# Kernel optimization log

Hardware: AMD Instinct MI355X
Metric: run time of the kernel (lower is better)

The kernel has to match this reference:

```python
import jax, jax.numpy as jnp
import numpy as np

T = 4096; D = 768; V = 32000; L = 4; EPS = 1e-5


def _ln(x, g, b):
    m = jnp.mean(x, axis=-1, keepdims=True)
    v = jnp.mean((x - m) ** 2, axis=-1, keepdims=True)
    return (x - m) * jax.lax.rsqrt(v + EPS) * g + b


def _qgelu(x):
    return x * jax.nn.sigmoid(1.702 * x)


def setup_inputs() -> dict:
    key = jax.random.key(0)
    ks = jax.random.split(key, 10)
    s = 0.02
    return {
        "idx": jax.random.randint(ks[0], (T,), 0, V),
        "wte": jax.random.normal(ks[1], (V, D)) * s,
        "rb_ln_g": jnp.ones((D,)), "rb_ln_b": jnp.zeros((D,)),
        "rb_fc_w": jax.random.normal(ks[2], (D, 4 * D)) * s,
        "rb_fc_b": jnp.zeros((4 * D,)),
        "rb_proj_w": jax.random.normal(ks[3], (4 * D, D)) * s,
        "rb_proj_b": jnp.zeros((D,)),
        "lnf_g": jnp.ones((D,)), "lnf_b": jnp.zeros((D,)),
        "lm_head_w": jax.random.normal(ks[4], (D, V)) * s,
        "mb_ln_g": jnp.ones((L, 2 * D)), "mb_ln_b": jnp.zeros((L, 2 * D)),
        "mb_fc_w": jax.random.normal(ks[5], (L, 2 * D, 4 * D)) * s,
        "mb_fc_b": jnp.zeros((L, 4 * D)),
        "mb_proj_w": jax.random.normal(ks[6], (L, 4 * D, D)) * s,
        "mb_proj_b": jnp.zeros((L, D)),
        "op_w": jax.random.normal(ks[7], (L, D, D)) * s,
        "op_b": jnp.zeros((L, D)),
        "lns_g": jnp.ones((L, D)), "lns_b": jnp.zeros((L, D)),
        "heads_w": jax.random.normal(ks[8], (L, D, V)) * s,
    }


def reference(idx, wte, rb_ln_g, rb_ln_b, rb_fc_w, rb_fc_b, rb_proj_w, rb_proj_b,
              lnf_g, lnf_b, lm_head_w, mb_ln_g, mb_ln_b, mb_fc_w, mb_fc_b,
              mb_proj_w, mb_proj_b, op_w, op_b, lns_g, lns_b, heads_w):
    # token embedding (dropout is identity in eval) + initial residual block
    x = wte[idx]  # [T, D]
    h = _ln(x, rb_ln_g, rb_ln_b)
    x = x + _qgelu(h @ rb_fc_w + rb_fc_b) @ rb_proj_w + rb_proj_b
    x = _ln(x, lnf_g, lnf_b)
    logits = x @ lm_head_w  # [T, V]

    # targets=None path: pred_targets = cat(idx[1:], [-1])
    pred_targets = jnp.concatenate([idx[1:], jnp.full((1,), -1, idx.dtype)])
    pos = jnp.arange(T)
    skey = jax.random.key(42)

    for i in range(L):  # static small loop over layers
        j = i + 1
        # multinomial(softmax(logits), 1) == categorical(logits)
        idx_next = jax.random.categorical(jax.random.fold_in(skey, i), logits)
        # positions p where the sample matched the next-token target and p < T - j
        mask = (idx_next == pred_targets) & (pos < T - j)  # [T] bool
        # x2[p] = x[p + j] (padded); compute merge densely, select with mask
        x2 = jnp.concatenate([x[j:], jnp.zeros((j, D), x.dtype)], axis=0)
        h = _ln(jnp.concatenate([x, x2], axis=-1), mb_ln_g[i], mb_ln_b[i])
        merged = x2 + _qgelu(h @ mb_fc_w[i] + mb_fc_b[i]) @ mb_proj_w[i] + mb_proj_b[i]
        # scatter merged[p] into x at position p + j where mask[p]
        merged_s = jnp.concatenate([jnp.zeros((j, D), x.dtype), merged[:-j]], axis=0)
        mask_s = jnp.concatenate([jnp.zeros((j,), bool), mask[:-j]], axis=0)
        x = jnp.where(mask_s[:, None], merged_s, x)
        x = x @ op_w[i] + op_b[i]
        x = _ln(x, lns_g[i], lns_b[i])
        logits = x @ heads_w[i]
    return logits
```

## Files before the change

### kernel.cpp

```cpp
#include <hip/hip_runtime.h>
#include <cstdint>
#include <cstddef>

#define T_TOK 4096
#define DIM   768
#define VOCAB 32000
#define NLAYER 4
#define HALF_TV 65536000u

typedef short bf16x8 __attribute__((ext_vector_type(8)));
typedef float f32x4  __attribute__((ext_vector_type(4)));
typedef float f32x4v __attribute__((ext_vector_type(4)));

__host__ __device__ inline void tf2x32(uint32_t k0, uint32_t k1, uint32_t& v0, uint32_t& v1){
  uint32_t ks2 = k0 ^ k1 ^ 0x1BD11BDAu;
  uint32_t x0 = v0 + k0, x1 = v1 + k1;
#define TFR(R) { x0 += x1; x1 = (x1<<R)|(x1>>(32-R)); x1 ^= x0; }
  TFR(13) TFR(15) TFR(26) TFR(6)
  x0 += k1;  x1 += ks2 + 1u;
  TFR(17) TFR(29) TFR(16) TFR(24)
  x0 += ks2; x1 += k0 + 2u;
  TFR(13) TFR(15) TFR(26) TFR(6)
  x0 += k0;  x1 += k1 + 3u;
  TFR(17) TFR(29) TFR(16) TFR(24)
  x0 += k1;  x1 += ks2 + 4u;
  TFR(13) TFR(15) TFR(26) TFR(6)
  x0 += ks2; x1 += k0 + 5u;
#undef TFR
  v0 = x0; v1 = x1;
}

__device__ inline float neglog_u(uint32_t k){
  float L;
  if (k >= 0x780000u){
    float x = (float)(0x800000u - k) * 1.1920928955078125e-7f;
    L = x * fmaf(x, fmaf(x, fmaf(x, 0.25f, 0.3333333333333f), 0.5f), 1.0f);
  } else {
    float l2k = __builtin_amdgcn_logf((float)k);
    L = 0.69314718055994531f * (23.0f - l2k);
    if (k == 0u) L = 87.33654475055310898f;
  }
  return L;
}

__device__ inline void gumbel_pair(uint32_t kf0, uint32_t kf1, uint32_t t_up, uint32_t v,
                                   float& gu, float& gd){
  uint32_t m = t_up * (uint32_t)VOCAB + v;
  uint32_t x0 = m, x1 = m + HALF_TV;
  tf2x32(kf0, kf1, x0, x1);
  float Lu = neglog_u(x0 >> 9);
  float Ld = neglog_u(x1 >> 9);
  gu = -0.69314718055994531f * __builtin_amdgcn_logf(Lu);
  gd = -0.69314718055994531f * __builtin_amdgcn_logf(Ld);
}

__device__ inline unsigned short f2bf(float f){
  uint32_t u = __float_as_uint(f);
  return (unsigned short)((u + 0x7FFFu + ((u >> 16) & 1u)) >> 16);
}
__device__ inline float bf2f(unsigned short h){
  return __uint_as_float(((uint32_t)h) << 16);
}
__device__ inline void cvt8(const float* f, bool lo, unsigned short* out){
  #pragma unroll
  for (int e=0;e<8;e++){
    float x = f[e];
    unsigned short h = f2bf(x);
    if (lo) h = f2bf(x - bf2f(h));
    out[e] = h;
  }
}
__device__ inline float blockReduceSum(float v){
  __shared__ float red[4];
  #pragma unroll
  for (int off=32; off>0; off>>=1) v += __shfl_down(v, off);
  int w = threadIdx.x >> 6;
  __syncthreads();
  if ((threadIdx.x & 63) == 0) red[w] = v;
  __syncthreads();
  return red[0] + red[1] + red[2] + red[3];
}

__device__ inline void gload16(const void* g, void* l){
  __builtin_amdgcn_global_load_lds(
      (const __attribute__((address_space(1))) unsigned int*)g,
      (__attribute__((address_space(3))) unsigned int*)l, 16, 0, 0);
}

enum { ST_F32 = 0, ST_HILO = 1, ST_SAMPLE = 2 };

template<int KSTEPS, int NSEG, int STORE, bool NTST, bool BIAS, bool QGELU>
__global__ __launch_bounds__(1024, 4) void k_hgemm256(
    const unsigned short* __restrict__ A0, const unsigned short* __restrict__ A1,
    const unsigned short* __restrict__ B0, const unsigned short* __restrict__ B2,
    float* __restrict__ C, unsigned short* __restrict__ Ch, unsigned short* __restrict__ Cl,
    const float* __restrict__ bias, uint32_t kf0, uint32_t kf1,
    unsigned long long* __restrict__ row_best, int N)
{
  constexpr int K  = KSTEPS * 64;
  constexpr int NT = NSEG * KSTEPS;
  __shared__ unsigned short sAll[65536];

  const int t = threadIdx.x;
  const int w = t >> 6, l = t & 63;
  const int wm = w >> 2, wn = w & 3;
  const int g = l >> 4, r = l & 15;

  int bid = blockIdx.x;
  int xcd = bid & 7, c = bid >> 3;
  int bm = xcd*2 + (c & 1);
  int bn = c >> 1;

  f32x4 acc[4][4] = {};

  size_t arow[2], brow[2];
  #pragma unroll
  for (int p=0;p<2;p++){
    int mr = p*128 + (t >> 3);
    int blk = mr >> 4;
    arow[p] = (size_t)(bm*128 + ((blk>>1)<<4) + (mr & 15) + ((blk & 1) ? 2048 : 0)) * K;
    int nr = p*128 + (t >> 3);
    brow[p] = (size_t)(bn*256 + nr) * K;
  }
  const int swz  = ((t & 7) ^ ((t >> 3) & 7)) << 3;
  const int ldst = t * 16;

  auto stage = [&](int vt){
    char* base = (char*)sAll + (vt & 1) * 65536;
    int seg = (NSEG == 1) ? 0 : (vt / KSTEPS);
    int k0  = ((NSEG == 1) ? vt : (vt % KSTEPS)) * 64;
    const unsigned short* Ap = (seg == 1) ? A1 : A0;
    const unsigned short* Bp = (seg == 2) ? B2 : B0;
    #pragma unroll
    for (int p=0;p<2;p++)
      gload16(Ap + arow[p] + k0 + swz, base + p*16384 + ldst);
    #pragma unroll
    for (int p=0;p<2;p++)
      gload16(Bp + brow[p] + k0 + swz, base + 32768 + p*16384 + ldst);
  };

  stage(0);
  __syncthreads();

  for (int vt = 0; vt < NT; ++vt){
    if (vt + 1 < NT) stage(vt + 1);
    const char* sA = (const char*)sAll + (vt & 1) * 65536;
    const char* sB = sA + 32768;
    #pragma unroll
    for (int kk=0;kk<2;kk++){
      bf16x8 bv[4], av[4];
      #pragma unroll
      for (int ni=0;ni<4;ni++){
        int tr = wn*64 + ni*16 + r;
        bv[ni] = *(const bf16x8*)(sB + tr*128 + (((kk*4+g) ^ (r&7))<<4));
      }
      #pragma unroll
      for (int q=0;q<4;q++){
        int tr = wm*64 + q*16 + r;
        av[q] = *(const bf16x8*)(sA + tr*128 + (((kk*4+g) ^ (r&7))<<4));
      }
      __builtin_amdgcn_s_setprio(1);
      #pragma unroll
      for (int q=0;q<4;q++)
        #pragma unroll
        for (int ni=0;ni<4;ni++)
          acc[q][ni] = __builtin_amdgcn_mfma_f32_16x16x32_bf16(av[q], bv[ni], acc[q][ni], 0, 0, 0);
      __builtin_amdgcn_s_setprio(0);
    }
    __syncthreads();
  }

  if constexpr (STORE == ST_SAMPLE){
    #pragma unroll
    for (int mi=0; mi<4; mi+=2){
      int row16 = (wm*2 + (mi>>1)) * 16;
      #pragma unroll
      for (int jj=0;jj<4;jj++){
        uint32_t t_up = bm*128 + row16 + g*4 + jj;
        unsigned long long bu = 0ull, bd = 0ull;
        #pragma unroll
        for (int ni=0;ni<4;ni++){
          uint32_t v = bn*256 + wn*64 + ni*16 + r;
          float gu, gd;
          gumbel_pair(kf0, kf1, t_up, v, gu, gd);
          float vu = acc[mi][ni][jj]   + gu;
          float vd = acc[mi+1][ni][jj] + gd;
          uint32_t fu = __float_as_uint(vu); fu = (fu & 0x80000000u) ? ~fu : (fu | 0x80000000u);
          uint32_t fd = __float_as_uint(vd); fd = (fd & 0x80000000u) ? ~fd : (fd | 0x80000000u);
          unsigned long long pu = ((unsigned long long)fu << 32) | (unsigned long long)(~v);
          unsigned long long pd = ((unsigned long long)fd << 32) | (unsigned long long)(~v);
          if (pu > bu) bu = pu;
          if (pd > bd) bd = pd;
        }
        #pragma unroll
        for (int off=1; off<16; off<<=1){
          unsigned int l0 = (unsigned int)bu, h0 = (unsigned int)(bu>>32);
          unsigned int l1 = __shfl_xor(l0, off), h1 = __shfl_xor(h0, off);
          unsigned long long o = ((unsigned long long)h1 << 32) | (unsigned long long)l1;
          if (o > bu) bu = o;
          l0 = (unsigned int)bd; h0 = (unsigned int)(bd>>32);
          l1 = __shfl_xor(l0, off); h1 = __shfl_xor(h0, off);
          o = ((unsigned long long)h1 << 32) | (unsigned long long)l1;
          if (o > bd) bd = o;
        }
        if (r == 0){
          atomicMax(&row_best[t_up], bu);
          atomicMax(&row_best[t_up + 2048], bd);
        }
      }
    }
  } else {
    #pragma unroll
    for (int mi=0;mi<4;mi++){
      int blk = wm*4 + mi;
      int mbase = bm*128 + ((blk>>1)<<4) + ((blk & 1) ? 2048 : 0);
      #pragma unroll
      for (int ni=0;ni<4;ni++){
        int n = bn*256 + wn*64 + ni*16 + r;
        float bv_ = BIAS ? bias[n] : 0.0f;
        #pragma unroll
        for (int jj=0;jj<4;jj++){
          int m = mbase + g*4 + jj;
          float v = acc[mi][ni][jj] + bv_;
          if constexpr (QGELU) v = v / (1.0f + expf(-1.702f * v));
          if constexpr (STORE == ST_F32){
            if constexpr (NTST) __builtin_nontemporal_store(v, &C[(size_t)m * N + n]);
            else                C[(size_t)m * N + n] = v;
          } else {
            unsigned short h = f2bf(v);
            Ch[(size_t)m * N + n] = h;
            Cl[(size_t)m * N + n] = f2bf(v - bf2f(h));
          }
        }
      }
    }
  }
}

template<int KSTEPS, int NSEG, bool BIAS, bool QGELU, bool RES, int STORE>
__global__ __launch_bounds__(256) void k_hgemm(
    const unsigned short* __restrict__ A0, const unsigned short* __restrict__ A1,
    const unsigned short* __restrict__ B0, const unsigned short* __restrict__ B2,
    float* __restrict__ C, unsigned short* __restrict__ Ch, unsigned short* __restrict__ Cl,
    const float* __restrict__ bias, const float* __restrict__ res,
    int N, uint32_t kf0, uint32_t kf1, unsigned long long* __restrict__ row_best)
{
  constexpr int K  = KSTEPS * 64;
  constexpr int NT = NSEG * KSTEPS;
  __shared__ unsigned short sAll[2 * 16 * 1024];

  const int t = threadIdx.x;
  const int wave = t >> 6, lane = t & 63;
  const int wm = wave >> 1, wn = wave & 1;
  const int g = lane >> 4, r = lane & 15;
  const int lr = lane >> 3, lc = lane & 7;

  int bid = blockIdx.x;
  int xcd = bid & 7, c = bid >> 3;
  int bm = xcd*4 + (c & 3);
  int bn = c >> 2;

  f32x4 acc[4][4] = {};

  size_t arow[4], brow[4];
  #pragma unroll
  for (int p=0;p<4;p++){
    int mr = p*32 + wave*8 + lr;
    int blk = mr >> 4;
    arow[p] = (size_t)(bm*64 + ((blk>>1)<<4) + (mr & 15) + ((blk & 1) ? 2048 : 0)) * K;
    brow[p] = (size_t)(bn*128 + mr) * K;
  }
  const int swz  = (lc ^ lr) << 3;
  const int ldst = (wave*8 + lr)*128 + lc*16;

  auto stage = [&](int vt){
    char* base = (char*)sAll + (vt & 1) * 32768;
    int seg = (NSEG == 1) ? 0 : (vt / KSTEPS);
    int k0  = ((NSEG == 1) ? vt : (vt % KSTEPS)) * 64;
    const unsigned short* Ap = (seg == 1) ? A1 : A0;
    const unsigned short* Bp = (seg == 2) ? B2 : B0;
    #pragma unroll
    for (int p=0;p<4;p++){
      gload16(Ap + arow[p] + k0 + swz, base + p*4096 + ldst);
      gload16(Bp + brow[p] + k0 + swz, base + 16384 + p*4096 + ldst);
    }
  };

  stage(0);
  __syncthreads();

  for (int vt = 0; vt < NT; ++vt){
    if (vt + 1 < NT) stage(vt + 1);
    const char* sA = (const char*)sAll + (vt & 1) * 32768;
    const char* sB = sA + 16384;
    #pragma unroll
    for (int kk=0;kk<2;kk++){
      bf16x8 av[4], bv[4];
      #pragma unroll
      for (int mi=0;mi<4;mi++){
        int tr = wm*64 + mi*16 + r;
        av[mi] = *(const bf16x8*)(sA + tr*128 + (((kk*4+g) ^ (r&7))<<4));
      }
      #pragma unroll
      for (int ni=0;ni<4;ni++){
        int tr = wn*64 + ni*16 + r;
        bv[ni] = *(const bf16x8*)(sB + tr*128 + (((kk*4+g) ^ (r&7))<<4));
      }
      #pragma unroll
      for (int mi=0;mi<4;mi++)
        #pragma unroll
        for (int ni=0;ni<4;ni++)
          acc[mi][ni] = __builtin_amdgcn_mfma_f32_16x16x32_bf16(av[mi], bv[ni], acc[mi][ni], 0, 0, 0);
    }
    __syncthreads();
  }

  #pragma unroll
  for (int mi=0;mi<4;mi++){
    int blk2 = wm*4 + mi;
    int mbase = bm*64 + ((blk2>>1)<<4) + ((blk2 & 1) ? 2048 : 0);
    #pragma unroll
    for (int ni=0;ni<4;ni++){
      int n = bn*128 + wn*64 + ni*16 + r;
      float bv_ = BIAS ? bias[n] : 0.0f;
      #pragma unroll
      for (int jj=0;jj<4;jj++){
        int m = mbase + g*4 + jj;
        float v = acc[mi][ni][jj] + bv_;
        if constexpr (QGELU) v = v / (1.0f + expf(-1.702f * v));
        if constexpr (RES)   v += res[(size_t)m * N + n];
        if constexpr (STORE == ST_F32){
          C[(size_t)m * N + n] = v;
        } else {
          unsigned short h = f2bf(v);
          Ch[(size_t)m * N + n] = h;
          Cl[(size_t)m * N + n] = f2bf(v - bf2f(h));
        }
      }
    }
  }
}

template<bool SPLIT>
__global__ __launch_bounds__(256) void k_wt_t(const float* __restrict__ W,
    unsigned short* __restrict__ Bh, unsigned short* __restrict__ Bl, int K, int N)
{
  __shared__ unsigned short sH[64][72];
  __shared__ unsigned short sL[64][72];
  int kt = blockIdx.x, nt = blockIdx.y;
  int t = threadIdx.x;
  int kr = t >> 4, nc4 = (t & 15) * 4;
  #pragma unroll
  for (int p=0;p<4;p++){
    int k = p*16 + kr;
    f32x4v w = __builtin_nontemporal_load((const f32x4v*)&W[(size_t)(kt*64 + k) * N + nt*64 + nc4]);
    #pragma unroll
    for (int e=0;e<4;e++){
      unsigned short h = f2bf(w[e]);
      sH[nc4+e][k] = h;
      if (SPLIT) sL[nc4+e][k] = f2bf(w[e] - bf2f(h));
    }
  }
  __syncthreads();
  #pragma unroll
  for (int q=0;q<2;q++){
    int cid = t + q*256;
    int n = cid >> 3, ch = cid & 7;
    *(bf16x8*)&Bh[(size_t)(nt*64+n)*K + kt*64 + ch*8] = *(const bf16x8*)&sH[n][ch*8];
    if (SPLIT)
      *(bf16x8*)&Bl[(size_t)(nt*64+n)*K + kt*64 + ch*8] = *(const bf16x8*)&sL[n][ch*8];
  }
}

__global__ __launch_bounds__(256) void k_embed_ln(const int* __restrict__ idx,
    const float* __restrict__ wte, const float* __restrict__ g, const float* __restrict__ b,
    float* __restrict__ Xraw, unsigned short* __restrict__ Hh, unsigned short* __restrict__ Hl)
{
  int row = blockIdx.x;
  const float* src = wte + (size_t)idx[row] * DIM;
  float v[3];
  #pragma unroll
  for (int jj=0;jj<3;jj++) v[jj] = src[threadIdx.x + jj*256];
  float s = blockReduceSum(v[0]+v[1]+v[2]);
  float mean = s * (1.0f/DIM);
  float s2 = 0;
  #pragma unroll
  for (int jj=0;jj<3;jj++){ float d = v[jj]-mean; s2 += d*d; }
  s2 = blockReduceSum(s2);
  float rs = rsqrtf(s2 * (1.0f/DIM) + 1e-5f);
  #pragma unroll
  for (int jj=0;jj<3;jj++){
    int d = threadIdx.x + jj*256;
    Xraw[(size_t)row*DIM + d] = v[jj];
    float o = (v[jj]-mean)*rs*g[d] + b[d];
    unsigned short h = f2bf(o);
    Hh[(size_t)row*DIM + d] = h;
    Hl[(size_t)row*DIM + d] = f2bf(o - bf2f(h));
  }
}

__global__ __launch_bounds__(256) void k_ln(const float* __restrict__ in, float* __restrict__ out,
    const float* __restrict__ g, const float* __restrict__ b,
    unsigned short* __restrict__ obf, unsigned short* __restrict__ olo)
{
  int row = blockIdx.x;
  const float* src = in + (size_t)row * DIM;
  float v[3];
  #pragma unroll
  for (int jj=0;jj<3;jj++) v[jj] = src[threadIdx.x + jj*256];
  float s = blockReduceSum(v[0]+v[1]+v[2]);
  float mean = s * (1.0f/DIM);
  float s2 = 0;
  #pragma unroll
  for (int jj=0;jj<3;jj++){ float d = v[jj]-mean; s2 += d*d; }
  s2 = blockReduceSum(s2);
  float rs = rsqrtf(s2 * (1.0f/DIM) + 1e-5f);
  #pragma unroll
  for (int jj=0;jj<3;jj++){
    int d = threadIdx.x + jj*256;
    float o = (v[jj]-mean)*rs*g[d] + b[d];
    out[(size_t)row*DIM + d] = o;
    unsigned short h = f2bf(o);
    obf[(size_t)row*DIM + d] = h;
    olo[(size_t)row*DIM + d] = f2bf(o - bf2f(h));
  }
}

__global__ void k_mask(const unsigned long long* __restrict__ row_best,
    const int* __restrict__ idx, int j, int* __restrict__ count, int* __restrict__ plist)
{
  int t = blockIdx.x * blockDim.x + threadIdx.x;
  if (t >= T_TOK) return;
  int v = (int)(~(uint32_t)(row_best[t] & 0xFFFFFFFFull));
  int tgt = (t < T_TOK-1) ? idx[t+1] : -1;
  if (v == tgt && t < T_TOK - j){
    int pos = atomicAdd(count, 1);
    plist[pos] = t;
  }
}

__global__ __launch_bounds__(256) void k_merge(const float* __restrict__ X,
    const int* __restrict__ plist, const int* __restrict__ count,
    const float* __restrict__ lng, const float* __restrict__ lnb,
    const float* __restrict__ fcw, const float* __restrict__ fcb,
    const float* __restrict__ pjw, const float* __restrict__ pjb,
    float* __restrict__ mergebuf, int j)
{
  __shared__ float sh[1536 + 3072];
  int nb = *count;
  for (int bIdx = blockIdx.x; bIdx < nb; bIdx += gridDim.x){
    int p = plist[bIdx];
    const float* xp = X + (size_t)p * DIM;
    const float* x2 = X + (size_t)(p + j) * DIM;
    for (int d = threadIdx.x; d < 1536; d += 256)
      sh[d] = (d < DIM) ? xp[d] : x2[d - DIM];
    __syncthreads();
    float s = 0;
    for (int d = threadIdx.x; d < 1536; d += 256) s += sh[d];
    s = blockReduceSum(s);
    float mean = s * (1.0f/1536.0f);
    float s2 = 0;
    for (int d = threadIdx.x; d < 1536; d += 256){ float df = sh[d]-mean; s2 += df*df; }
    s2 = blockReduceSum(s2);
    float rs = rsqrtf(s2 * (1.0f/1536.0f) + 1e-5f);
    __syncthreads();
    for (int d = threadIdx.x; d < 1536; d += 256)
      sh[d] = (sh[d]-mean)*rs*lng[d] + lnb[d];
    __syncthreads();
    float* act = sh + 1536;
    #pragma unroll
    for (int jj=0;jj<12;jj++){
      int n = threadIdx.x + jj*256;
      float a = fcb[n];
      for (int k=0;k<1536;k++) a += sh[k]*fcw[(size_t)k*3072 + n];
      act[n] = a / (1.0f + expf(-1.702f*a));
    }
    __syncthreads();
    #pragma unroll
    for (int jj=0;jj<3;jj++){
      int d = threadIdx.x + jj*256;
      float a = pjb[d];
      for (int k=0;k<3072;k++) a += act[k]*pjw[(size_t)k*DIM + d];
      mergebuf[(size_t)bIdx*DIM + d] = x2[d] + a;
    }
    __syncthreads();
  }
}

__global__ void k_scatter(float* __restrict__ X, unsigned short* __restrict__ Xbf,
    unsigned short* __restrict__ Xlo, const float* __restrict__ mergebuf,
    const int* __restrict__ plist, const int* __restrict__ count, int j)
{
  int nb = *count;
  for (int bIdx = blockIdx.x; bIdx < nb; bIdx += gridDim.x){
    int p = plist[bIdx];
    for (int d = threadIdx.x; d < DIM; d += 256){
      float v = mergebuf[(size_t)bIdx*DIM + d];
      size_t o = (size_t)(p + j)*DIM + d;
      X[o] = v;
      unsigned short h = f2bf(v);
      Xbf[o] = h;
      Xlo[o] = f2bf(v - bf2f(h));
    }
  }
}

__global__ __launch_bounds__(256) void k_gemm_old(
    const float* __restrict__ A, const float* __restrict__ B, float* __restrict__ C,
    int M, int N, int K)
{
  __shared__ unsigned short sA[128*64];
  __shared__ unsigned short sB[128*64];
  const int t = threadIdx.x;
  const int bn = blockIdx.x, bm = blockIdx.y;
  const int wave = t >> 6, lane = t & 63;
  const int wm = wave >> 1, wn = wave & 1;
  const int g = lane >> 4, r = lane & 15;
  f32x4 acc[4][4] = {};
  const int nK = K >> 6;
  const int aC = t & 7,  aM0 = t >> 3;
  const int bN0 = t & 31, bC = t >> 5;
  const float* Abase = A + (size_t)(bm*128) * K;
  const float* Bbase = B + (size_t)(bn*128);
  for (int seg = 0; seg < 3; ++seg) {
    const bool aLO = (seg == 1), bLO = (seg == 2);
    for (int kb = 0; kb < nK; ++kb) {
      const int k0 = kb << 6;
      __syncthreads();
      #pragma unroll
      for (int p=0;p<4;p++){
        int m = p*32 + aM0;
        const float* src = Abase + (size_t)m * K + k0 + aC*8;
        float ff[8];
        *(float4*)(ff)   = *(const float4*)(src);
        *(float4*)(ff+4) = *(const float4*)(src+4);
        unsigned short hh[8];
        cvt8(ff, aLO, hh);
        *(bf16x8*)&sA[m*64 + ((aC ^ (m & 7)) * 8)] = *(bf16x8*)hh;
      }
      #pragma unroll
      for (int p=0;p<4;p++){
        int n = p*32 + bN0;
        float ff[8];
        const float* src = Bbase + (size_t)(k0 + bC*8) * N + n;
        #pragma unroll
        for (int e=0;e<8;e++) ff[e] = src[(size_t)e * N];
        unsigned short hh[8];
        cvt8(ff, bLO, hh);
        *(bf16x8*)&sB[n*64 + ((bC ^ (n & 7)) * 8)] = *(bf16x8*)hh;
      }
      __syncthreads();
      #pragma unroll
      for (int kk=0;kk<2;kk++){
        bf16x8 av[4], bv[4];
        #pragma unroll
        for (int mi=0;mi<4;mi++){
          int m = wm*64 + mi*16 + r;
          av[mi] = *(const bf16x8*)&sA[m*64 + (((kk*4 + g) ^ (m & 7)) * 8)];
        }
        #pragma unroll
        for (int ni=0;ni<4;ni++){
          int n = wn*64 + ni*16 + r;
          bv[ni] = *(const bf16x8*)&sB[n*64 + (((kk*4 + g) ^ (n & 7)) * 8)];
        }
        #pragma unroll
        for (int mi=0;mi<4;mi++)
          #pragma unroll
          for (int ni=0;ni<4;ni++)
            acc[mi][ni] = __builtin_amdgcn_mfma_f32_16x16x32_bf16(av[mi], bv[ni], acc[mi][ni], 0, 0, 0);
      }
    }
  }
  #pragma unroll
  for (int mi=0;mi<4;mi++)
    #pragma unroll
    for (int ni=0;ni<4;ni++)
      #pragma unroll
      for (int jj=0;jj<4;jj++){
        int m = bm*128 + wm*64 + mi*16 + g*4 + jj;
        int n = bn*128 + wn*64 + ni*16 + r;
        C[(size_t)m * N + n] = acc[mi][ni][jj];
      }
}

static void fold_key(uint32_t i, uint32_t& o0, uint32_t& o1){
  uint32_t x0 = 0, x1 = i;
  tf2x32(0u, 42u, x0, x1);
  o0 = x0; o1 = x1;
}

extern "C" void kernel_launch(void* const* d_in, const int* in_sizes, int n_in,
                              void* d_out, int out_size, void* d_ws, size_t ws_size,
                              hipStream_t stream)
{
  const int*   idx       = (const int*)  d_in[0];
  const float* wte       = (const float*)d_in[1];
  const float* rb_ln_g   = (const float*)d_in[2];
  const float* rb_ln_b   = (const float*)d_in[3];
  const float* rb_fc_w   = (const float*)d_in[4];
  const float* rb_fc_b   = (const float*)d_in[5];
  const float* rb_proj_w = (const float*)d_in[6];
  const float* rb_proj_b = (const float*)d_in[7];
  const float* lnf_g     = (const float*)d_in[8];
  const float* lnf_b     = (const float*)d_in[9];
  const float* lm_head_w = (const float*)d_in[10];
  const float* mb_ln_g   = (const float*)d_in[11];
  const float* mb_ln_b   = (const float*)d_in[12];
  const float* mb_fc_w   = (const float*)d_in[13];
  const float* mb_fc_b   = (const float*)d_in[14];
  const float* mb_proj_w = (const float*)d_in[15];
  const float* mb_proj_b = (const float*)d_in[16];
  const float* op_w      = (const float*)d_in[17];
  const float* op_b      = (const float*)d_in[18];
  const float* lns_g     = (const float*)d_in[19];
  const float* lns_b     = (const float*)d_in[20];
  const float* heads_w   = (const float*)d_in[21];

  const size_t TD = (size_t)T_TOK * DIM;
  const size_t DV = (size_t)DIM * VOCAB;

  float* X = (float*)d_ws;
  float* Y = X + TD;
  unsigned short* Xbf = (unsigned short*)(Y + TD);
  unsigned short* Xlo = Xbf + TD;
  unsigned short* BtFh = Xlo + TD;
  unsigned short* BtFl = BtFh + DV;
  size_t need_big = (size_t)((char*)(BtFl + DV) - (char*)d_ws);
  bool big = ws_size >= need_big;

  char* ob = (char*)d_out;
  float* OUT = (float*)d_out;
  unsigned short* Hh     = (unsigned short*)(ob);
  unsigned short* Hl     = Hh + TD;
  unsigned short* ACTh   = (unsigned short*)(ob + ((size_t)16<<20));
  unsigned short* ACTl   = ACTh + TD*4;
  unsigned short* Btfc_h = (unsigned short*)(ob + ((size_t)72<<20));
  unsigned short* Btfc_l = Btfc_h + (size_t)3072*DIM;
  unsigned short* Btpj_h = (unsigned short*)(ob + ((size_t)84<<20));
  unsigned short* Btpj_l = Btpj_h + (size_t)3072*DIM;
  unsigned short* BtS    = (unsigned short*)(ob + ((size_t)96<<20));
  unsigned short* Btop_h = (unsigned short*)(ob + ((size_t)152<<20));
  unsigned short* Btop_l = Btop_h + (size_t)DIM*DIM;
  float* MERGE = (float*)(ob + ((size_t)160<<20));
  unsigned long long* ROWBEST = (unsigned long long*)(ob + ((size_t)176<<20));
  int* COUNT = (int*)(ROWBEST + T_TOK);
  int* PLIST = COUNT + 1;

  dim3 blk(256);
  dim3 blk16(1024);

  k_embed_ln<<<T_TOK, blk, 0, stream>>>(idx, wte, rb_ln_g, rb_ln_b, X, Hh, Hl);
  k_wt_t<true><<<dim3(12,48), blk, 0, stream>>>(rb_fc_w,   Btfc_h, Btfc_l, DIM,  3072);
  k_wt_t<true><<<dim3(48,12), blk, 0, stream>>>(rb_proj_w, Btpj_h, Btpj_l, 3072, DIM);
  k_hgemm256<12,3,ST_HILO,false,true,true><<<16*12, blk16, 0, stream>>>(
      Hh, Hl, Btfc_h, Btfc_l, nullptr, ACTh, ACTl, rb_fc_b, 0u,0u, nullptr, 3072);
  k_hgemm<48,3,true,false,true,ST_F32><<<6*32, blk, 0, stream>>>(
      ACTh, ACTl, Btpj_h, Btpj_l, Y, nullptr, nullptr, rb_proj_b, X, DIM, 0u,0u, nullptr);
  k_ln<<<T_TOK, blk, 0, stream>>>(Y, X, lnf_g, lnf_b, Xbf, Xlo);

  for (int i = 0; i < NLAYER; ++i){
    int j = i + 1;
    uint32_t kf0, kf1; fold_key((uint32_t)i, kf0, kf1);

    hipMemsetAsync(ROWBEST, 0, (size_t)T_TOK*8 + 4, stream);

    const float* hw = (i == 0) ? lm_head_w : heads_w + (size_t)(i-1)*DV;
    k_wt_t<false><<<dim3(12,500), blk, 0, stream>>>(hw, BtS, nullptr, DIM, VOCAB);
    k_hgemm256<12,1,ST_SAMPLE,false,false,false><<<2000, blk16, 0, stream>>>(
        Xbf, Xbf, BtS, BtS, nullptr, nullptr, nullptr, nullptr, kf0, kf1, ROWBEST, VOCAB);

    k_mask<<<T_TOK/256, blk, 0, stream>>>(ROWBEST, idx, j, COUNT, PLIST);
    k_merge<<<64, blk, 0, stream>>>(X, PLIST, COUNT,
        mb_ln_g + (size_t)i*1536, mb_ln_b + (size_t)i*1536,
        mb_fc_w + (size_t)i*1536*3072, mb_fc_b + (size_t)i*3072,
        mb_proj_w + (size_t)i*3072*DIM, mb_proj_b + (size_t)i*DIM, MERGE, j);
    k_scatter<<<64, blk, 0, stream>>>(X, Xbf, Xlo, MERGE, PLIST, COUNT, j);

    k_wt_t<true><<<dim3(12,12), blk, 0, stream>>>(op_w + (size_t)i*DIM*DIM, Btop_h, Btop_l, DIM, DIM);
    k_hgemm<12,3,true,false,false,ST_F32><<<6*32, blk, 0, stream>>>(
        Xbf, Xlo, Btop_h, Btop_l, Y, nullptr, nullptr, op_b + (size_t)i*DIM, nullptr,
        DIM, 0u,0u, nullptr);
    k_ln<<<T_TOK, blk, 0, stream>>>(Y, X, lns_g + (size_t)i*DIM, lns_b + (size_t)i*DIM, Xbf, Xlo);
  }

  if (big){
    k_wt_t<true><<<dim3(12,500), blk, 0, stream>>>(heads_w + (size_t)3*DV, BtFh, BtFl, DIM, VOCAB);
    k_hgemm256<12,3,ST_F32,true,false,false><<<2000, blk16, 0, stream>>>(
        Xbf, Xlo, BtFh, BtFl, OUT, nullptr, nullptr, nullptr, 0u, 0u, nullptr, VOCAB);
  } else {
    k_gemm_old<<<dim3(VOCAB/128, T_TOK/128), blk, 0, stream>>>(
        X, heads_w + (size_t)3*DV, OUT, T_TOK, VOCAB, DIM);
  }
}
```

Before: 2.564 ms.

## Use 8-wave blocks with 128x64 warp tiles and barrier-interleaved MFMA phases

```diff
diff --git a/kernel.cpp b/kernel.cpp
--- a/kernel.cpp
+++ b/kernel.cpp
@@ -90,7 +90,7 @@
 enum { ST_F32 = 0, ST_HILO = 1, ST_SAMPLE = 2 };
 
 template<int KSTEPS, int NSEG, int STORE, bool NTST, bool BIAS, bool QGELU>
-__global__ __launch_bounds__(1024, 4) void k_hgemm256(
+__global__ __launch_bounds__(512, 2) void k_hgemm256(
     const unsigned short* __restrict__ A0, const unsigned short* __restrict__ A1,
     const unsigned short* __restrict__ B0, const unsigned short* __restrict__ B2,
     float* __restrict__ C, unsigned short* __restrict__ Ch, unsigned short* __restrict__ Cl,
@@ -105,25 +105,29 @@
   const int w = t >> 6, l = t & 63;
   const int wm = w >> 2, wn = w & 3;
   const int g = l >> 4, r = l & 15;
+  const int lr = l >> 3, lc = l & 7;
 
   int bid = blockIdx.x;
   int xcd = bid & 7, c = bid >> 3;
   int bm = xcd*2 + (c & 1);
   int bn = c >> 1;
 
-  f32x4 acc[4][4] = {};
-
-  size_t arow[2], brow[2];
-  #pragma unroll
-  for (int p=0;p<2;p++){
-    int mr = p*128 + (t >> 3);
+  f32x4 acc[8][4] = {};
+
+  int grow[8];
+  #pragma unroll
+  for (int p=0;p<4;p++){
+    int mr = p*64 + w*8 + lr;
     int blk = mr >> 4;
-    arow[p] = (size_t)(bm*128 + ((blk>>1)<<4) + (mr & 15) + ((blk & 1) ? 2048 : 0)) * K;
-    int nr = p*128 + (t >> 3);
-    brow[p] = (size_t)(bn*256 + nr) * K;
-  }
-  const int swz  = ((t & 7) ^ ((t >> 3) & 7)) << 3;
-  const int ldst = t * 16;
+    grow[p] = (bm*128 + ((blk>>1)<<4) + (mr & 15) + ((blk & 1) ? 2048 : 0)) * K;
+  }
+  #pragma unroll
+  for (int p=0;p<4;p++){
+    int nr = p*64 + w*8 + lr;
+    grow[4+p] = (bn*256 + nr) * K;
+  }
+  const int swz  = (lc ^ lr) << 3;
+  const int ldst = (w*8)*128 + l*16;
 
   auto stage = [&](int vt){
     char* base = (char*)sAll + (vt & 1) * 65536;
@@ -132,11 +136,11 @@
     const unsigned short* Ap = (seg == 1) ? A1 : A0;
     const unsigned short* Bp = (seg == 2) ? B2 : B0;
     #pragma unroll
-    for (int p=0;p<2;p++)
-      gload16(Ap + arow[p] + k0 + swz, base + p*16384 + ldst);
-    #pragma unroll
-    for (int p=0;p<2;p++)
-      gload16(Bp + brow[p] + k0 + swz, base + 32768 + p*16384 + ldst);
+    for (int p=0;p<4;p++)
+      gload16(Ap + (size_t)(grow[p] + k0) + swz, base + p*8192 + ldst);
+    #pragma unroll
+    for (int p=0;p<4;p++)
+      gload16(Bp + (size_t)(grow[4+p] + k0) + swz, base + 32768 + p*8192 + ldst);
   };
 
   stage(0);
@@ -146,34 +150,44 @@
     if (vt + 1 < NT) stage(vt + 1);
     const char* sA = (const char*)sAll + (vt & 1) * 65536;
     const char* sB = sA + 32768;
+    bf16x8 av[4], bv[4];
     #pragma unroll
     for (int kk=0;kk<2;kk++){
-      bf16x8 bv[4], av[4];
-      #pragma unroll
-      for (int ni=0;ni<4;ni++){
-        int tr = wn*64 + ni*16 + r;
-        bv[ni] = *(const bf16x8*)(sB + tr*128 + (((kk*4+g) ^ (r&7))<<4));
-      }
-      #pragma unroll
-      for (int q=0;q<4;q++){
-        int tr = wm*64 + q*16 + r;
-        av[q] = *(const bf16x8*)(sA + tr*128 + (((kk*4+g) ^ (r&7))<<4));
-      }
-      __builtin_amdgcn_s_setprio(1);
-      #pragma unroll
-      for (int q=0;q<4;q++)
-        #pragma unroll
-        for (int ni=0;ni<4;ni++)
-          acc[q][ni] = __builtin_amdgcn_mfma_f32_16x16x32_bf16(av[q], bv[ni], acc[q][ni], 0, 0, 0);
-      __builtin_amdgcn_s_setprio(0);
+      #pragma unroll
+      for (int mh=0; mh<2; mh++){
+        if (mh == 0){
+          #pragma unroll
+          for (int ni=0;ni<4;ni++){
+            int tr = wn*64 + ni*16 + r;
+            bv[ni] = *(const bf16x8*)(sB + tr*128 + (((kk*4+g) ^ (r&7))<<4));
+          }
+        }
+        #pragma unroll
+        for (int q=0;q<4;q++){
+          int tr = wm*128 + (mh*4+q)*16 + r;
+          av[q] = *(const bf16x8*)(sA + tr*128 + (((kk*4+g) ^ (r&7))<<4));
+        }
+        __builtin_amdgcn_s_barrier();
+        asm volatile("s_waitcnt lgkmcnt(0)" ::: "memory");
+        __builtin_amdgcn_sched_barrier(0);
+        __builtin_amdgcn_s_setprio(1);
+        #pragma unroll
+        for (int q=0;q<4;q++)
+          #pragma unroll
+          for (int ni=0;ni<4;ni++)
+            acc[mh*4+q][ni] = __builtin_amdgcn_mfma_f32_16x16x32_bf16(av[q], bv[ni], acc[mh*4+q][ni], 0, 0, 0);
+        __builtin_amdgcn_s_setprio(0);
+        __builtin_amdgcn_s_barrier();
+      }
     }
     __syncthreads();
   }
 
   if constexpr (STORE == ST_SAMPLE){
     #pragma unroll
-    for (int mi=0; mi<4; mi+=2){
-      int row16 = (wm*2 + (mi>>1)) * 16;
+    for (int mi=0; mi<8; mi+=2){
+      int blk = wm*8 + mi;
+      int row16 = (blk>>1) << 4;
       #pragma unroll
       for (int jj=0;jj<4;jj++){
         uint32_t t_up = bm*128 + row16 + g*4 + jj;
@@ -211,8 +225,8 @@
     }
   } else {
     #pragma unroll
-    for (int mi=0;mi<4;mi++){
-      int blk = wm*4 + mi;
+    for (int mi=0;mi<8;mi++){
+      int blk = wm*8 + mi;
       int mbase = bm*128 + ((blk>>1)<<4) + ((blk & 1) ? 2048 : 0);
       #pragma unroll
       for (int ni=0;ni<4;ni++){
@@ -647,12 +661,12 @@
   int* PLIST = COUNT + 1;
 
   dim3 blk(256);
-  dim3 blk16(1024);
+  dim3 blk8(512);
 
   k_embed_ln<<<T_TOK, blk, 0, stream>>>(idx, wte, rb_ln_g, rb_ln_b, X, Hh, Hl);
   k_wt_t<true><<<dim3(12,48), blk, 0, stream>>>(rb_fc_w,   Btfc_h, Btfc_l, DIM,  3072);
   k_wt_t<true><<<dim3(48,12), blk, 0, stream>>>(rb_proj_w, Btpj_h, Btpj_l, 3072, DIM);
-  k_hgemm256<12,3,ST_HILO,false,true,true><<<16*12, blk16, 0, stream>>>(
+  k_hgemm256<12,3,ST_HILO,false,true,true><<<16*12, blk8, 0, stream>>>(
       Hh, Hl, Btfc_h, Btfc_l, nullptr, ACTh, ACTl, rb_fc_b, 0u,0u, nullptr, 3072);
   k_hgemm<48,3,true,false,true,ST_F32><<<6*32, blk, 0, stream>>>(
       ACTh, ACTl, Btpj_h, Btpj_l, Y, nullptr, nullptr, rb_proj_b, X, DIM, 0u,0u, nullptr);
@@ -666,7 +680,7 @@
 
     const float* hw = (i == 0) ? lm_head_w : heads_w + (size_t)(i-1)*DV;
     k_wt_t<false><<<dim3(12,500), blk, 0, stream>>>(hw, BtS, nullptr, DIM, VOCAB);
-    k_hgemm256<12,1,ST_SAMPLE,false,false,false><<<2000, blk16, 0, stream>>>(
+    k_hgemm256<12,1,ST_SAMPLE,false,false,false><<<2000, blk8, 0, stream>>>(
         Xbf, Xbf, BtS, BtS, nullptr, nullptr, nullptr, nullptr, kf0, kf1, ROWBEST, VOCAB);
 
     k_mask<<<T_TOK/256, blk, 0, stream>>>(ROWBEST, idx, j, COUNT, PLIST);
@@ -685,7 +699,7 @@
 
   if (big){
     k_wt_t<true><<<dim3(12,500), blk, 0, stream>>>(heads_w + (size_t)3*DV, BtFh, BtFl, DIM, VOCAB);
-    k_hgemm256<12,3,ST_F32,true,false,false><<<2000, blk16, 0, stream>>>(
+    k_hgemm256<12,3,ST_F32,true,false,false><<<2000, blk8, 0, stream>>>(
         Xbf, Xlo, BtFh, BtFl, OUT, nullptr, nullptr, nullptr, 0u, 0u, nullptr, VOCAB);
   } else {
     k_gemm_old<<<dim3(VOCAB/128, T_TOK/128), blk, 0, stream>>>(
```

Result: slower. 2.843 ms (+10.9%).

## Make big GEMM persistent and split small GEMMs by segment with fused reduce-LN

Applied to the files above, without the earlier changes.

```diff
diff --git a/kernel.cpp b/kernel.cpp
--- a/kernel.cpp
+++ b/kernel.cpp
@@ -95,7 +95,7 @@
     const unsigned short* __restrict__ B0, const unsigned short* __restrict__ B2,
     float* __restrict__ C, unsigned short* __restrict__ Ch, unsigned short* __restrict__ Cl,
     const float* __restrict__ bias, uint32_t kf0, uint32_t kf1,
-    unsigned long long* __restrict__ row_best, int N)
+    unsigned long long* __restrict__ row_best, int N, int SMAX)
 {
   constexpr int K  = KSTEPS * 64;
   constexpr int NT = NSEG * KSTEPS;
@@ -106,26 +106,22 @@
   const int wm = w >> 2, wn = w & 3;
   const int g = l >> 4, r = l & 15;
 
-  int bid = blockIdx.x;
-  int xcd = bid & 7, c = bid >> 3;
-  int bm = xcd*2 + (c & 1);
-  int bn = c >> 1;
-
-  f32x4 acc[4][4] = {};
-
-  size_t arow[2], brow[2];
+  const int xcd  = blockIdx.x & 7;
+  const int nloc = gridDim.x >> 3;
+  const int lcl  = blockIdx.x >> 3;
+
+  int abase[2], nbase[2];
   #pragma unroll
   for (int p=0;p<2;p++){
     int mr = p*128 + (t >> 3);
     int blk = mr >> 4;
-    arow[p] = (size_t)(bm*128 + ((blk>>1)<<4) + (mr & 15) + ((blk & 1) ? 2048 : 0)) * K;
-    int nr = p*128 + (t >> 3);
-    brow[p] = (size_t)(bn*256 + nr) * K;
+    abase[p] = ((blk>>1)<<4) + (mr & 15) + ((blk & 1) ? 2048 : 0);
+    nbase[p] = p*128 + (t >> 3);
   }
   const int swz  = ((t & 7) ^ ((t >> 3) & 7)) << 3;
   const int ldst = t * 16;
 
-  auto stage = [&](int vt){
+  auto stage = [&](int vt, int bm_, int bn_){
     char* base = (char*)sAll + (vt & 1) * 65536;
     int seg = (NSEG == 1) ? 0 : (vt / KSTEPS);
     int k0  = ((NSEG == 1) ? vt : (vt % KSTEPS)) * 64;
@@ -133,120 +129,133 @@
     const unsigned short* Bp = (seg == 2) ? B2 : B0;
     #pragma unroll
     for (int p=0;p<2;p++)
-      gload16(Ap + arow[p] + k0 + swz, base + p*16384 + ldst);
+      gload16(Ap + (size_t)(bm_*128 + abase[p]) * K + k0 + swz, base + p*16384 + ldst);
     #pragma unroll
     for (int p=0;p<2;p++)
-      gload16(Bp + brow[p] + k0 + swz, base + 32768 + p*16384 + ldst);
+      gload16(Bp + (size_t)(bn_*256 + nbase[p]) * K + k0 + swz, base + 32768 + p*16384 + ldst);
   };
 
-  stage(0);
+  int s = lcl;
+  if (s >= SMAX) return;
+  int bm = xcd*2 + (s & 1), bn = s >> 1;
+  stage(0, bm, bn);
   __syncthreads();
 
-  for (int vt = 0; vt < NT; ++vt){
-    if (vt + 1 < NT) stage(vt + 1);
-    const char* sA = (const char*)sAll + (vt & 1) * 65536;
-    const char* sB = sA + 32768;
-    #pragma unroll
-    for (int kk=0;kk<2;kk++){
-      bf16x8 bv[4], av[4];
-      #pragma unroll
-      for (int ni=0;ni<4;ni++){
-        int tr = wn*64 + ni*16 + r;
-        bv[ni] = *(const bf16x8*)(sB + tr*128 + (((kk*4+g) ^ (r&7))<<4));
-      }
-      #pragma unroll
-      for (int q=0;q<4;q++){
-        int tr = wm*64 + q*16 + r;
-        av[q] = *(const bf16x8*)(sA + tr*128 + (((kk*4+g) ^ (r&7))<<4));
-      }
-      __builtin_amdgcn_s_setprio(1);
-      #pragma unroll
-      for (int q=0;q<4;q++)
-        #pragma unroll
-        for (int ni=0;ni<4;ni++)
-          acc[q][ni] = __builtin_amdgcn_mfma_f32_16x16x32_bf16(av[q], bv[ni], acc[q][ni], 0, 0, 0);
-      __builtin_amdgcn_s_setprio(0);
-    }
-    __syncthreads();
-  }
-
-  if constexpr (STORE == ST_SAMPLE){
-    #pragma unroll
-    for (int mi=0; mi<4; mi+=2){
-      int row16 = (wm*2 + (mi>>1)) * 16;
-      #pragma unroll
-      for (int jj=0;jj<4;jj++){
-        uint32_t t_up = bm*128 + row16 + g*4 + jj;
-        unsigned long long bu = 0ull, bd = 0ull;
+  while (true) {
+    f32x4 acc[4][4] = {};
+    for (int vt = 0; vt < NT; ++vt){
+      if (vt + 1 < NT) stage(vt + 1, bm, bn);
+      const char* sA = (const char*)sAll + (vt & 1) * 65536;
+      const char* sB = sA + 32768;
+      #pragma unroll
+      for (int kk=0;kk<2;kk++){
+        bf16x8 bv[4], av[4];
         #pragma unroll
         for (int ni=0;ni<4;ni++){
-          uint32_t v = bn*256 + wn*64 + ni*16 + r;
-          float gu, gd;
-          gumbel_pair(kf0, kf1, t_up, v, gu, gd);
-          float vu = acc[mi][ni][jj]   + gu;
-          float vd = acc[mi+1][ni][jj] + gd;
-          uint32_t fu = __float_as_uint(vu); fu = (fu & 0x80000000u) ? ~fu : (fu | 0x80000000u);
-          uint32_t fd = __float_as_uint(vd); fd = (fd & 0x80000000u) ? ~fd : (fd | 0x80000000u);
-          unsigned long long pu = ((unsigned long long)fu << 32) | (unsigned long long)(~v);
-          unsigned long long pd = ((unsigned long long)fd << 32) | (unsigned long long)(~v);
-          if (pu > bu) bu = pu;
-          if (pd > bd) bd = pd;
+          int tr = wn*64 + ni*16 + r;
+          bv[ni] = *(const bf16x8*)(sB + tr*128 + (((kk*4+g) ^ (r&7))<<4));
         }
         #pragma unroll
-        for (int off=1; off<16; off<<=1){
-          unsigned int l0 = (unsigned int)bu, h0 = (unsigned int)(bu>>32);
-          unsigned int l1 = __shfl_xor(l0, off), h1 = __shfl_xor(h0, off);
-          unsigned long long o = ((unsigned long long)h1 << 32) | (unsigned long long)l1;
-          if (o > bu) bu = o;
-          l0 = (unsigned int)bd; h0 = (unsigned int)(bd>>32);
-          l1 = __shfl_xor(l0, off); h1 = __shfl_xor(h0, off);
-          o = ((unsigned long long)h1 << 32) | (unsigned long long)l1;
-          if (o > bd) bd = o;
+        for (int q=0;q<4;q++){
+          int tr = wm*64 + q*16 + r;
+          av[q] = *(const bf16x8*)(sA + tr*128 + (((kk*4+g) ^ (r&7))<<4));
         }
-        if (r == 0){
-          atomicMax(&row_best[t_up], bu);
-          atomicMax(&row_best[t_up + 2048], bd);
-        }
-      }
-    }
-  } else {
-    #pragma unroll
-    for (int mi=0;mi<4;mi++){
-      int blk = wm*4 + mi;
-      int mbase = bm*128 + ((blk>>1)<<4) + ((blk & 1) ? 2048 : 0);
-      #pragma unroll
-      for (int ni=0;ni<4;ni++){
-        int n = bn*256 + wn*64 + ni*16 + r;
-        float bv_ = BIAS ? bias[n] : 0.0f;
+        __builtin_amdgcn_s_setprio(1);
+        #pragma unroll
+        for (int q=0;q<4;q++)
+          #pragma unroll
+          for (int ni=0;ni<4;ni++)
+            acc[q][ni] = __builtin_amdgcn_mfma_f32_16x16x32_bf16(av[q], bv[ni], acc[q][ni], 0, 0, 0);
+        __builtin_amdgcn_s_setprio(0);
+      }
+      __syncthreads();
+    }
+
+    int ns = s + nloc;
+    bool more = (ns < SMAX);
+    int nbm = 0, nbn = 0;
+    if (more){ nbm = xcd*2 + (ns & 1); nbn = ns >> 1; stage(0, nbm, nbn); }
+
+    if constexpr (STORE == ST_SAMPLE){
+      #pragma unroll
+      for (int mi=0; mi<4; mi+=2){
+        int row16 = (wm*2 + (mi>>1)) * 16;
         #pragma unroll
         for (int jj=0;jj<4;jj++){
-          int m = mbase + g*4 + jj;
-          float v = acc[mi][ni][jj] + bv_;
-          if constexpr (QGELU) v = v / (1.0f + expf(-1.702f * v));
-          if constexpr (STORE == ST_F32){
-            if constexpr (NTST) __builtin_nontemporal_store(v, &C[(size_t)m * N + n]);
-            else                C[(size_t)m * N + n] = v;
-          } else {
-            unsigned short h = f2bf(v);
-            Ch[(size_t)m * N + n] = h;
-            Cl[(size_t)m * N + n] = f2bf(v - bf2f(h));
+          uint32_t t_up = bm*128 + row16 + g*4 + jj;
+          unsigned long long bu = 0ull, bd = 0ull;
+          #pragma unroll
+          for (int ni=0;ni<4;ni++){
+            uint32_t v = bn*256 + wn*64 + ni*16 + r;
+            float gu, gd;
+            gumbel_pair(kf0, kf1, t_up, v, gu, gd);
+            float vu = acc[mi][ni][jj]   + gu;
+            float vd = acc[mi+1][ni][jj] + gd;
+            uint32_t fu = __float_as_uint(vu); fu = (fu & 0x80000000u) ? ~fu : (fu | 0x80000000u);
+            uint32_t fd = __float_as_uint(vd); fd = (fd & 0x80000000u) ? ~fd : (fd | 0x80000000u);
+            unsigned long long pu = ((unsigned long long)fu << 32) | (unsigned long long)(~v);
+            unsigned long long pd = ((unsigned long long)fd << 32) | (unsigned long long)(~v);
+            if (pu > bu) bu = pu;
+            if (pd > bd) bd = pd;
+          }
+          #pragma unroll
+          for (int off=1; off<16; off<<=1){
+            unsigned int l0 = (unsigned int)bu, h0 = (unsigned int)(bu>>32);
+            unsigned int l1 = __shfl_xor(l0, off), h1 = __shfl_xor(h0, off);
+            unsigned long long o = ((unsigned long long)h1 << 32) | (unsigned long long)l1;
+            if (o > bu) bu = o;
+            l0 = (unsigned int)bd; h0 = (unsigned int)(bd>>32);
+            l1 = __shfl_xor(l0, off); h1 = __shfl_xor(h0, off);
+            o = ((unsigned long long)h1 << 32) | (unsigned long long)l1;
+            if (o > bd) bd = o;
+          }
+          if (r == 0){
+            atomicMax(&row_best[t_up], bu);
+            atomicMax(&row_best[t_up + 2048], bd);
           }
         }
       }
-    }
-  }
-}
-
-template<int KSTEPS, int NSEG, bool BIAS, bool QGELU, bool RES, int STORE>
-__global__ __launch_bounds__(256) void k_hgemm(
-    const unsigned short* __restrict__ A0, const unsigned short* __restrict__ A1,
-    const unsigned short* __restrict__ B0, const unsigned short* __restrict__ B2,
-    float* __restrict__ C, unsigned short* __restrict__ Ch, unsigned short* __restrict__ Cl,
-    const float* __restrict__ bias, const float* __restrict__ res,
-    int N, uint32_t kf0, uint32_t kf1, unsigned long long* __restrict__ row_best)
+    } else {
+      #pragma unroll
+      for (int mi=0;mi<4;mi++){
+        int fb = wm*4 + mi;
+        int mbase = bm*128 + ((fb>>1)<<4) + ((fb & 1) ? 2048 : 0);
+        #pragma unroll
+        for (int ni=0;ni<4;ni++){
+          int n = bn*256 + wn*64 + ni*16 + r;
+          float bv_ = BIAS ? bias[n] : 0.0f;
+          #pragma unroll
+          for (int jj=0;jj<4;jj++){
+            int m = mbase + g*4 + jj;
+            float v = acc[mi][ni][jj] + bv_;
+            if constexpr (QGELU) v = v / (1.0f + expf(-1.702f * v));
+            if constexpr (STORE == ST_F32){
+              if constexpr (NTST) __builtin_nontemporal_store(v, &C[(size_t)m * N + n]);
+              else                C[(size_t)m * N + n] = v;
+            } else {
+              unsigned short h = f2bf(v);
+              Ch[(size_t)m * N + n] = h;
+              Cl[(size_t)m * N + n] = f2bf(v - bf2f(h));
+            }
+          }
+        }
+      }
+    }
+
+    if (!more) return;
+    __syncthreads();
+    s = ns; bm = nbm; bn = nbn;
+  }
+}
+
+template<int KSTEPS>
+__global__ __launch_bounds__(256) void k_hgemm_seg(
+    const unsigned short* __restrict__ Ah, const unsigned short* __restrict__ Al,
+    const unsigned short* __restrict__ Bh, const unsigned short* __restrict__ Bl,
+    float* __restrict__ Part, int N)
 {
   constexpr int K  = KSTEPS * 64;
-  constexpr int NT = NSEG * KSTEPS;
+  constexpr int NT = KSTEPS;
   __shared__ unsigned short sAll[2 * 16 * 1024];
 
   const int t = threadIdx.x;
@@ -255,7 +264,13 @@
   const int g = lane >> 4, r = lane & 15;
   const int lr = lane >> 3, lc = lane & 7;
 
-  int bid = blockIdx.x;
+  int bps = (N >> 7) * 32;
+  int seg = blockIdx.x / bps;
+  int bid = blockIdx.x % bps;
+  const unsigned short* Ap = (seg == 1) ? Al : Ah;
+  const unsigned short* Bp = (seg == 2) ? Bl : Bh;
+  float* C = Part + (size_t)seg * T_TOK * N;
+
   int xcd = bid & 7, c = bid >> 3;
   int bm = xcd*4 + (c & 3);
   int bn = c >> 2;
@@ -275,10 +290,7 @@
 
   auto stage = [&](int vt){
     char* base = (char*)sAll + (vt & 1) * 32768;
-    int seg = (NSEG == 1) ? 0 : (vt / KSTEPS);
-    int k0  = ((NSEG == 1) ? vt : (vt % KSTEPS)) * 64;
-    const unsigned short* Ap = (seg == 1) ? A1 : A0;
-    const unsigned short* Bp = (seg == 2) ? B2 : B0;
+    int k0 = vt * 64;
     #pragma unroll
     for (int p=0;p<4;p++){
       gload16(Ap + arow[p] + k0 + swz, base + p*4096 + ldst);
@@ -322,22 +334,49 @@
     #pragma unroll
     for (int ni=0;ni<4;ni++){
       int n = bn*128 + wn*64 + ni*16 + r;
-      float bv_ = BIAS ? bias[n] : 0.0f;
       #pragma unroll
       for (int jj=0;jj<4;jj++){
         int m = mbase + g*4 + jj;
-        float v = acc[mi][ni][jj] + bv_;
-        if constexpr (QGELU) v = v / (1.0f + expf(-1.702f * v));
-        if constexpr (RES)   v += res[(size_t)m * N + n];
-        if constexpr (STORE == ST_F32){
-          C[(size_t)m * N + n] = v;
-        } else {
-          unsigned short h = f2bf(v);
-          Ch[(size_t)m * N + n] = h;
-          Cl[(size_t)m * N + n] = f2bf(v - bf2f(h));
-        }
-      }
-    }
+        C[(size_t)m * N + n] = acc[mi][ni][jj];
+      }
+    }
+  }
+}
+
+__global__ __launch_bounds__(256) void k_redln(
+    const float* __restrict__ P, const float* __restrict__ bias,
+    const float* __restrict__ res,
+    const float* __restrict__ g, const float* __restrict__ b,
+    float* __restrict__ X, unsigned short* __restrict__ Xbf,
+    unsigned short* __restrict__ Xlo)
+{
+  const size_t TD1 = (size_t)T_TOK * DIM;
+  int row = blockIdx.x;
+  float v[3];
+  #pragma unroll
+  for (int jj=0;jj<3;jj++){
+    int d = threadIdx.x + jj*256;
+    size_t o = (size_t)row*DIM + d;
+    float x = P[o] + P[TD1 + o] + P[2*TD1 + o] + bias[d];
+    if (res) x += res[o];
+    v[jj] = x;
+  }
+  float s = blockReduceSum(v[0]+v[1]+v[2]);
+  float mean = s * (1.0f/DIM);
+  float s2 = 0;
+  #pragma unroll
+  for (int jj=0;jj<3;jj++){ float d = v[jj]-mean; s2 += d*d; }
+  s2 = blockReduceSum(s2);
+  float rs = rsqrtf(s2 * (1.0f/DIM) + 1e-5f);
+  #pragma unroll
+  for (int jj=0;jj<3;jj++){
+    int d = threadIdx.x + jj*256;
+    size_t o = (size_t)row*DIM + d;
+    float out = (v[jj]-mean)*rs*g[d] + b[d];
+    X[o] = out;
+    unsigned short h = f2bf(out);
+    Xbf[o] = h;
+    Xlo[o] = f2bf(out - bf2f(h));
   }
 }
 
@@ -396,33 +435,6 @@
     unsigned short h = f2bf(o);
     Hh[(size_t)row*DIM + d] = h;
     Hl[(size_t)row*DIM + d] = f2bf(o - bf2f(h));
-  }
-}
-
-__global__ __launch_bounds__(256) void k_ln(const float* __restrict__ in, float* __restrict__ out,
-    const float* __restrict__ g, const float* __restrict__ b,
-    unsigned short* __restrict__ obf, unsigned short* __restrict__ olo)
-{
-  int row = blockIdx.x;
-  const float* src = in + (size_t)row * DIM;
-  float v[3];
-  #pragma unroll
-  for (int jj=0;jj<3;jj++) v[jj] = src[threadIdx.x + jj*256];
-  float s = blockReduceSum(v[0]+v[1]+v[2]);
-  float mean = s * (1.0f/DIM);
-  float s2 = 0;
-  #pragma unroll
-  for (int jj=0;jj<3;jj++){ float d = v[jj]-mean; s2 += d*d; }
-  s2 = blockReduceSum(s2);
-  float rs = rsqrtf(s2 * (1.0f/DIM) + 1e-5f);
-  #pragma unroll
-  for (int jj=0;jj<3;jj++){
-    int d = threadIdx.x + jj*256;
-    float o = (v[jj]-mean)*rs*g[d] + b[d];
-    out[(size_t)row*DIM + d] = o;
-    unsigned short h = f2bf(o);
-    obf[(size_t)row*DIM + d] = h;
-    olo[(size_t)row*DIM + d] = f2bf(o - bf2f(h));
   }
 }
 
@@ -645,6 +657,7 @@
   unsigned long long* ROWBEST = (unsigned long long*)(ob + ((size_t)176<<20));
   int* COUNT = (int*)(ROWBEST + T_TOK);
   int* PLIST = COUNT + 1;
+  float* PART = (float*)(ob + ((size_t)192<<20));
 
   dim3 blk(256);
   dim3 blk16(1024);
@@ -652,11 +665,10 @@
   k_embed_ln<<<T_TOK, blk, 0, stream>>>(idx, wte, rb_ln_g, rb_ln_b, X, Hh, Hl);
   k_wt_t<true><<<dim3(12,48), blk, 0, stream>>>(rb_fc_w,   Btfc_h, Btfc_l, DIM,  3072);
   k_wt_t<true><<<dim3(48,12), blk, 0, stream>>>(rb_proj_w, Btpj_h, Btpj_l, 3072, DIM);
-  k_hgemm256<12,3,ST_HILO,false,true,true><<<16*12, blk16, 0, stream>>>(
-      Hh, Hl, Btfc_h, Btfc_l, nullptr, ACTh, ACTl, rb_fc_b, 0u,0u, nullptr, 3072);
-  k_hgemm<48,3,true,false,true,ST_F32><<<6*32, blk, 0, stream>>>(
-      ACTh, ACTl, Btpj_h, Btpj_l, Y, nullptr, nullptr, rb_proj_b, X, DIM, 0u,0u, nullptr);
-  k_ln<<<T_TOK, blk, 0, stream>>>(Y, X, lnf_g, lnf_b, Xbf, Xlo);
+  k_hgemm256<12,3,ST_HILO,false,true,true><<<192, blk16, 0, stream>>>(
+      Hh, Hl, Btfc_h, Btfc_l, nullptr, ACTh, ACTl, rb_fc_b, 0u,0u, nullptr, 3072, 24);
+  k_hgemm_seg<48><<<576, blk, 0, stream>>>(ACTh, ACTl, Btpj_h, Btpj_l, PART, DIM);
+  k_redln<<<T_TOK, blk, 0, stream>>>(PART, rb_proj_b, X, lnf_g, lnf_b, X, Xbf, Xlo);
 
   for (int i = 0; i < NLAYER; ++i){
     int j = i + 1;
@@ -666,8 +678,8 @@
 
     const float* hw = (i == 0) ? lm_head_w : heads_w + (size_t)(i-1)*DV;
     k_wt_t<false><<<dim3(12,500), blk, 0, stream>>>(hw, BtS, nullptr, DIM, VOCAB);
-    k_hgemm256<12,1,ST_SAMPLE,false,false,false><<<2000, blk16, 0, stream>>>(
-        Xbf, Xbf, BtS, BtS, nullptr, nullptr, nullptr, nullptr, kf0, kf1, ROWBEST, VOCAB);
+    k_hgemm256<12,1,ST_SAMPLE,false,false,false><<<512, blk16, 0, stream>>>(
+        Xbf, Xbf, BtS, BtS, nullptr, nullptr, nullptr, nullptr, kf0, kf1, ROWBEST, VOCAB, 250);
 
     k_mask<<<T_TOK/256, blk, 0, stream>>>(ROWBEST, idx, j, COUNT, PLIST);
     k_merge<<<64, blk, 0, stream>>>(X, PLIST, COUNT,
@@ -677,16 +689,15 @@
     k_scatter<<<64, blk, 0, stream>>>(X, Xbf, Xlo, MERGE, PLIST, COUNT, j);
 
     k_wt_t<true><<<dim3(12,12), blk, 0, stream>>>(op_w + (size_t)i*DIM*DIM, Btop_h, Btop_l, DIM, DIM);
-    k_hgemm<12,3,true,false,false,ST_F32><<<6*32, blk, 0, stream>>>(
-        Xbf, Xlo, Btop_h, Btop_l, Y, nullptr, nullptr, op_b + (size_t)i*DIM, nullptr,
-        DIM, 0u,0u, nullptr);
-    k_ln<<<T_TOK, blk, 0, stream>>>(Y, X, lns_g + (size_t)i*DIM, lns_b + (size_t)i*DIM, Xbf, Xlo);
+    k_hgemm_seg<12><<<576, blk, 0, stream>>>(Xbf, Xlo, Btop_h, Btop_l, PART, DIM);
+    k_redln<<<T_TOK, blk, 0, stream>>>(PART, op_b + (size_t)i*DIM, nullptr,
+        lns_g + (size_t)i*DIM, lns_b + (size_t)i*DIM, X, Xbf, Xlo);
   }
 
   if (big){
     k_wt_t<true><<<dim3(12,500), blk, 0, stream>>>(heads_w + (size_t)3*DV, BtFh, BtFl, DIM, VOCAB);
-    k_hgemm256<12,3,ST_F32,true,false,false><<<2000, blk16, 0, stream>>>(
-        Xbf, Xlo, BtFh, BtFl, OUT, nullptr, nullptr, nullptr, 0u, 0u, nullptr, VOCAB);
+    k_hgemm256<12,3,ST_F32,true,false,false><<<512, blk16, 0, stream>>>(
+        Xbf, Xlo, BtFh, BtFl, OUT, nullptr, nullptr, nullptr, 0u, 0u, nullptr, VOCAB, 250);
   } else {
     k_gemm_old<<<dim3(VOCAB/128, T_TOK/128), blk, 0, stream>>>(
         X, heads_w + (size_t)3*DV, OUT, T_TOK, VOCAB, DIM);
```

Measured after the change: 2.496 ms, median of 3. 1.03x faster.
